# Optimization experiments

Hardware: AMD Instinct MI355X
Metric: run time of the kernel (lower is better)

## Reference

```python
import jax, jax.numpy as jnp
import numpy as np

H = 2048          # hidden_size
I = 2048          # per-expert intermediate = 6144 // (topk=2 + share=1)
E_ROUTED = 7      # num_experts - num_share_experts
NS = 1            # num_share_experts
TOPK = 2
TEMP = 1.0


def setup_inputs() -> dict:
    key = jax.random.key(0)
    ks = jax.random.split(key, 20)
    s = lambda fan_in: 1.0 / np.sqrt(fan_in)
    inp = {
        "x": jax.random.normal(ks[0], (4, 1024, H), dtype=jnp.float32),
        # router (nn.Linear(H, E_ROUTED)) + learnable gate bias (init zeros)
        "Wr": jax.random.normal(ks[1], (H, E_ROUTED), jnp.float32) * s(H),
        "br": jax.random.normal(ks[2], (E_ROUTED,), jnp.float32) * s(H),
        "gate_bias": jnp.zeros((E_ROUTED,), jnp.float32),
        # stacked routed-expert FFN params (up -> SwiGLU gate -> down)
        "Wup": jax.random.normal(ks[3], (E_ROUTED, H, I), jnp.float32) * s(H),
        "bup": jax.random.normal(ks[4], (E_ROUTED, I), jnp.float32) * s(H),
        "Wgate": jax.random.normal(ks[5], (E_ROUTED, I, I), jnp.float32) * s(I),
        "bgate": jax.random.normal(ks[6], (E_ROUTED, I), jnp.float32) * s(I),
        "Wdown": jax.random.normal(ks[7], (E_ROUTED, I, H), jnp.float32) * s(I),
        "bdown": jax.random.normal(ks[8], (E_ROUTED, H), jnp.float32) * s(I),
        # shared expert: share_up Linear(H, NS*I), SwiGLU(I), share_down Linear(I, H)
        "Wsu": jax.random.normal(ks[9], (H, NS * I), jnp.float32) * s(H),
        "bsu": jax.random.normal(ks[10], (NS * I,), jnp.float32) * s(H),
        "Wsg": jax.random.normal(ks[11], (I, I), jnp.float32) * s(I),
        "bsg": jax.random.normal(ks[12], (I,), jnp.float32) * s(I),
        "Wsd": jax.random.normal(ks[13], (I, H), jnp.float32) * s(I),
        "bsd": jax.random.normal(ks[14], (H,), jnp.float32) * s(I),
    }
    return inp


def _moe_forward(x, Wr, br, gate_bias, Wup, bup, Wgate, bgate, Wdown, bdown,
                 Wsu, bsu, Wsg, bsg, Wsd, bsd):
    B, S, _ = x.shape
    xt = x.reshape(-1, H)                                   # [N, H]
    N = xt.shape[0]

    # ---- router: top-k gating with scatter(-inf) + softmax over all routed experts
    gate = (xt @ Wr + br) / TEMP                            # [N, E]
    bias_gate = gate + gate_bias
    _, ids = jax.lax.top_k(bias_gate, TOPK)                 # [N, K]
    sel_logits = jnp.take_along_axis(gate, ids, axis=-1)    # [N, K] (unbiased logits)
    masked = jnp.full_like(gate, -jnp.inf)
    masked = masked.at[jnp.arange(N)[:, None], ids].set(sel_logits)
    probs = jax.nn.softmax(masked, axis=-1)                 # [N, E], zero off top-k

    # ---- routed experts: dense grouped FFN, combine weighted by probs
    # (probs are exactly 0 for unselected experts, matching the masked
    #  gather / scatter-add combine in the original loop)
    u = jnp.einsum('nh,ehi->eni', xt, Wup) + bup[:, None, :]            # [E, N, I]
    g = jax.nn.silu(jnp.einsum('eni,eij->enj', u, Wgate) + bgate[:, None, :]) * u
    eo = jnp.einsum('enj,ejh->enh', g, Wdown) + bdown[:, None, :]       # [E, N, H]
    out = jnp.einsum('ne,enh->nh', probs, eo)                           # [N, H]

    # ---- shared expert(s)
    su = (xt @ Wsu + bsu).reshape(N, NS, I)                 # [N, NS, I]
    sg = jax.nn.silu(su @ Wsg + bsg) * su                   # SwiGLU
    so = (sg @ Wsd + bsd).sum(axis=1)                       # [N, H]
    out = out + so

    return out.reshape(B, S, H)


def reference(x, Wr, br, gate_bias, Wup, bup, Wgate, bgate, Wdown, bdown,
              Wsu, bsu, Wsg, bsg, Wsd, bsd):
    return _moe_forward(x, Wr, br, gate_bias, Wup, bup, Wgate, bgate,
                        Wdown, bdown, Wsu, bsu, Wsg, bsg, Wsd, bsd)
```

## Files before the change

kernel.cpp:

```cpp
#include <hip/hip_runtime.h>
#include <stdint.h>

#define HD 2048
#define NTOK 4096
#define NROUTED 7
#define NEXP 8
#define ROWS_ROUTED 8192
#define ROWS_TOTAL 12288
#define ROWS_PAD 12416

#define BM 256
#define BN 256
#define BK 32
#define NT (HD / BK)

typedef __attribute__((ext_vector_type(8))) __bf16 bf16x8;
typedef __attribute__((ext_vector_type(4))) float f32x4;
typedef __attribute__((ext_vector_type(8))) unsigned short u16x8;

__device__ __forceinline__ float bf2f(unsigned short h) {
  union { unsigned int u; float f; } x; x.u = ((unsigned int)h) << 16; return x.f;
}
__device__ __forceinline__ unsigned short f2bf(float f) {
  union { float f; unsigned int u; } x; x.f = f;
  unsigned int r = x.u + 0x7fffu + ((x.u >> 16) & 1u);
  return (unsigned short)(r >> 16);
}

__device__ __forceinline__ void async16(const void* g, void* l) {
  __builtin_amdgcn_global_load_lds(
      (__attribute__((address_space(1))) const void*)(uintptr_t)g,
      (__attribute__((address_space(3))) void*)(unsigned int)(uintptr_t)l,
      16, 0, 0);
}

__global__ __launch_bounds__(256) void k_convert_bf16(const float* __restrict__ in,
                                                      unsigned short* __restrict__ out, int n) {
  int i = (blockIdx.x * 256 + threadIdx.x) * 4;
  if (i >= n) return;
  float4 v = *(const float4*)(in + i);
  ushort4 o; o.x = f2bf(v.x); o.y = f2bf(v.y); o.z = f2bf(v.z); o.w = f2bf(v.w);
  *(ushort4*)(out + i) = o;
}

__global__ __launch_bounds__(256) void k_transpose_bf16(const float* __restrict__ in,
                                                        unsigned short* __restrict__ out) {
  __shared__ float tile[64][65];
  const size_t bs = (size_t)HD * HD;
  in += (size_t)blockIdx.z * bs; out += (size_t)blockIdx.z * bs;
  int tx = threadIdx.x & 15, ty = threadIdx.x >> 4;
  int r0 = blockIdx.y * 64, c0 = blockIdx.x * 64;
  #pragma unroll
  for (int i = 0; i < 4; i++) {
    float4 v = *(const float4*)(in + (size_t)(r0 + ty + 16 * i) * HD + c0 + tx * 4);
    tile[ty + 16 * i][tx * 4 + 0] = v.x;
    tile[ty + 16 * i][tx * 4 + 1] = v.y;
    tile[ty + 16 * i][tx * 4 + 2] = v.z;
    tile[ty + 16 * i][tx * 4 + 3] = v.w;
  }
  __syncthreads();
  #pragma unroll
  for (int i = 0; i < 4; i++) {
    int orow = ty + 16 * i;
    int oc = tx * 4;
    ushort4 o;
    o.x = f2bf(tile[oc + 0][orow]);
    o.y = f2bf(tile[oc + 1][orow]);
    o.z = f2bf(tile[oc + 2][orow]);
    o.w = f2bf(tile[oc + 3][orow]);
    *(ushort4*)(out + (size_t)(c0 + orow) * HD + r0 + oc) = o;
  }
}

__global__ __launch_bounds__(256) void k_router(const float* __restrict__ x, const float* __restrict__ Wr,
                                                const float* __restrict__ br, const float* __restrict__ gbias,
                                                int* __restrict__ ids, float* __restrict__ wts,
                                                int* __restrict__ ctrl) {
  int lane = threadIdx.x & 63, wid = threadIdx.x >> 6;
  int t = blockIdx.x * 4 + wid;
  const float* xr = x + (size_t)t * HD;
  float acc[NROUTED];
  #pragma unroll
  for (int e = 0; e < NROUTED; e++) acc[e] = 0.f;
  for (int k = lane; k < HD; k += 64) {
    float xv = xr[k];
    const float* wrow = Wr + k * NROUTED;
    #pragma unroll
    for (int e = 0; e < NROUTED; e++) acc[e] += xv * wrow[e];
  }
  #pragma unroll
  for (int e = 0; e < NROUTED; e++) {
    #pragma unroll
    for (int off = 32; off > 0; off >>= 1) acc[e] += __shfl_down(acc[e], off);
  }
  if (lane == 0) {
    float lg[NROUTED], bg[NROUTED];
    #pragma unroll
    for (int e = 0; e < NROUTED; e++) { lg[e] = acc[e] + br[e]; bg[e] = lg[e] + gbias[e]; }
    int i1 = 0;
    #pragma unroll
    for (int e = 1; e < NROUTED; e++) if (bg[e] > bg[i1]) i1 = e;
    int i2 = (i1 == 0) ? 1 : 0;
    #pragma unroll
    for (int e = 0; e < NROUTED; e++) if (e != i1 && bg[e] > bg[i2]) i2 = e;
    float l1 = lg[i1], l2 = lg[i2];
    float m = fmaxf(l1, l2);
    float p1 = __expf(l1 - m), p2 = __expf(l2 - m);
    float s = p1 + p2;
    ids[2*t] = i1; ids[2*t+1] = i2;
    wts[2*t] = p1 / s; wts[2*t+1] = p2 / s;
    atomicAdd(&ctrl[i1], 1); atomicAdd(&ctrl[i2], 1);
  }
}

__global__ void k_offsets(int* ctrl) {
  if (threadIdx.x == 0 && blockIdx.x == 0) {
    ctrl[7] = NTOK;
    int o = 0;
    #pragma unroll
    for (int e = 0; e < NEXP; e++) { ctrl[8 + e] = o; o += ctrl[e]; }
  }
}

__global__ __launch_bounds__(256) void k_build_lists(const int* __restrict__ ids, int* __restrict__ ctrl,
                                                     int* __restrict__ tok_list, int* __restrict__ tok_pos) {
  int t = blockIdx.x * 256 + threadIdx.x;
  if (t >= NTOK) return;
  #pragma unroll
  for (int j = 0; j < 2; j++) {
    int e = ids[2*t + j];
    int pos = ctrl[8 + e] + atomicAdd(&ctrl[16 + e], 1);
    tok_list[pos] = t;
    tok_pos[2*t + j] = pos;
  }
  tok_list[ROWS_ROUTED + t] = t;
}


#define STAGE(bufp)                                                       \
  { unsigned short* _a = &sm[bufp][0][0];                                 \
    unsigned short* _b = &sm[bufp][1][0];                                 \
    _Pragma("unroll")                                                     \
    for (int r = 0; r < 2; r++) {                                         \
      async16(pA[r], _a + r * 4096 + wid * 512); pA[r] += BK;             \
      async16(pB[r], _b + r * 4096 + wid * 512); pB[r] += BK;             \
    } }

template<int MODE>
__global__ __launch_bounds__(512, 2) void k_moe_gemm(
    const unsigned short* __restrict__ Abase,
    const unsigned short* __restrict__ WTr,
    const unsigned short* __restrict__ WTs,
    const float* __restrict__ biasR,
    const float* __restrict__ biasS,
    const int* __restrict__ ctrl,
    const int* __restrict__ tok_list,
    const unsigned short* __restrict__ Uep,
    unsigned short* __restrict__ Out)
{
  const int e   = blockIdx.z;
  const int cnt = ctrl[e];
  const int m0  = blockIdx.y * BM;
  if (m0 >= cnt) return;
  const int off = ctrl[8 + e];
  const int n0  = blockIdx.x * BN;

  const unsigned short* W = (e < NROUTED) ? (WTr + (size_t)e * HD * HD) : WTs;
  const float* bias = (e < NROUTED) ? (biasR + e * HD) : biasS;

  __shared__ __align__(16) unsigned short sm[2][2][BM * BK];

  const int tid  = threadIdx.x;
  const int lane = tid & 63;
  const int wid  = tid >> 6;

  const int sc  = tid & 3;
  const int rl  = tid >> 2;
  const int csw = (sc ^ (rl & 3)) * 8;
  const unsigned short* pA[2];
  const unsigned short* pB[2];
  #pragma unroll
  for (int r = 0; r < 2; r++) {
    int row = r * 128 + rl;
    size_t ga;
    if (MODE == 0) {
      int mr = m0 + row; if (mr >= cnt) mr = cnt - 1;
      ga = (size_t)tok_list[off + mr] * HD;
    } else {
      ga = (size_t)(off + m0 + row) * HD;
    }
    pA[r] = Abase + ga + csw;
    pB[r] = W + (size_t)(n0 + row) * HD + csw;
  }

  const int wr   = wid >> 2;
  const int wc   = wid & 3;
  const int rm   = lane & 15;
  const int q    = lane >> 4;
  const int sw   = rm & 3;
  const int aRow = wr * 128 + rm;
  const int bRow = wc * 64 + rm;

  f32x4 acc[8][4];
  f32x4 zero = {0.f, 0.f, 0.f, 0.f};
  #pragma unroll
  for (int i = 0; i < 8; i++)
    #pragma unroll
    for (int j = 0; j < 4; j++) acc[i][j] = zero;

  STAGE(0);
  __syncthreads();

  for (int t = 0; t < NT; ++t) {
    const int buf = t & 1;
    if (t + 1 < NT) STAGE(buf ^ 1);

    const unsigned short* _ab = &sm[buf][0][0];
    const unsigned short* _bb = &sm[buf][1][0];
    bf16x8 af[8], bf[4];
    #pragma unroll
    for (int mi = 0; mi < 8; mi++)
      af[mi] = *(const bf16x8*)(_ab + (aRow + mi * 16) * BK + ((q ^ sw) * 8));
    #pragma unroll
    for (int ni = 0; ni < 4; ni++)
      bf[ni] = *(const bf16x8*)(_bb + (bRow + ni * 16) * BK + ((q ^ sw) * 8));
    #pragma unroll
    for (int mi = 0; mi < 8; mi++)
      #pragma unroll
      for (int ni = 0; ni < 4; ni++)
        acc[mi][ni] = __builtin_amdgcn_mfma_f32_16x16x32_bf16(af[mi], bf[ni], acc[mi][ni], 0, 0, 0);

    __syncthreads();
  }

  #pragma unroll
  for (int mi = 0; mi < 8; mi++) {
    int rb = wr * 128 + mi * 16 + q * 4;
    #pragma unroll
    for (int r = 0; r < 4; r++) {
      int gm = m0 + rb + r;
      if (gm < cnt) {
        size_t orow = (size_t)(off + gm) * HD;
        #pragma unroll
        for (int ni = 0; ni < 4; ni++) {
          int gn = n0 + wc * 64 + ni * 16 + rm;
          float v = acc[mi][ni][r] + bias[gn];
          if (MODE == 1) {
            float uv = bf2f(Uep[orow + gn]);
            float sg = v / (1.f + __expf(-v));
            v = sg * uv;
          }
          Out[orow + gn] = f2bf(v);
        }
      }
    }
  }
}

__global__ __launch_bounds__(256) void k_combine(const unsigned short* __restrict__ eo,
                                                 const int* __restrict__ tok_pos,
                                                 const float* __restrict__ wts,
                                                 float* __restrict__ out) {
  int t = blockIdx.x;
  int h = threadIdx.x * 8;
  int p0 = tok_pos[2*t], p1 = tok_pos[2*t+1];
  float w0 = wts[2*t], w1 = wts[2*t+1];
  u16x8 a = *(const u16x8*)(eo + (size_t)p0 * HD + h);
  u16x8 b = *(const u16x8*)(eo + (size_t)p1 * HD + h);
  u16x8 c = *(const u16x8*)(eo + (size_t)(ROWS_ROUTED + t) * HD + h);
  float* o = out + (size_t)t * HD + h;
  #pragma unroll
  for (int i = 0; i < 8; i++) o[i] = w0 * bf2f(a[i]) + w1 * bf2f(b[i]) + bf2f(c[i]);
}

extern "C" void kernel_launch(void* const* d_in, const int* in_sizes, int n_in,
                              void* d_out, int out_size, void* d_ws, size_t ws_size,
                              hipStream_t stream) {
  (void)in_sizes; (void)n_in; (void)out_size; (void)ws_size;
  const float* x     = (const float*)d_in[0];
  const float* Wr    = (const float*)d_in[1];
  const float* br    = (const float*)d_in[2];
  const float* gbias = (const float*)d_in[3];
  const float* Wup   = (const float*)d_in[4];
  const float* bup   = (const float*)d_in[5];
  const float* Wgate = (const float*)d_in[6];
  const float* bgate = (const float*)d_in[7];
  const float* Wdown = (const float*)d_in[8];
  const float* bdown = (const float*)d_in[9];
  const float* Wsu   = (const float*)d_in[10];
  const float* bsu   = (const float*)d_in[11];
  const float* Wsg   = (const float*)d_in[12];
  const float* bsg   = (const float*)d_in[13];
  const float* Wsd   = (const float*)d_in[14];
  const float* bsd   = (const float*)d_in[15];
  float* out = (float*)d_out;

  char* ws = (char*)d_ws;
  size_t o = 0;
  auto alloc = [&](size_t bytes) { char* p = ws + o; o += (bytes + 255) & ~(size_t)255; return p; };
  unsigned short* WT_r = (unsigned short*)alloc((size_t)7 * HD * HD * 2);
  unsigned short* WT_s = (unsigned short*)alloc((size_t)HD * HD * 2);
  unsigned short* xbf  = (unsigned short*)alloc((size_t)NTOK * HD * 2);
  unsigned short* bufU = (unsigned short*)alloc((size_t)ROWS_PAD * HD * 2);
  unsigned short* bufG = (unsigned short*)alloc((size_t)ROWS_PAD * HD * 2);
  int*   ctrl     = (int*)alloc(4096);
  int*   ids      = (int*)alloc(NTOK * 2 * 4);
  float* wts      = (float*)alloc(NTOK * 2 * 4);
  int*   tok_list = (int*)alloc(ROWS_TOTAL * 4);
  int*   tok_pos  = (int*)alloc(NTOK * 2 * 4);

  hipMemsetAsync(ctrl, 0, 96, stream);
  k_convert_bf16<<<NTOK * HD / 1024, 256, 0, stream>>>(x, xbf, NTOK * HD);
  k_router<<<NTOK / 4, 256, 0, stream>>>(x, Wr, br, gbias, ids, wts, ctrl);
  k_offsets<<<1, 64, 0, stream>>>(ctrl);
  k_build_lists<<<NTOK / 256, 256, 0, stream>>>(ids, ctrl, tok_list, tok_pos);

  dim3 tgrid(HD / 64, HD / 64, 7), tgrid1(HD / 64, HD / 64, 1);
  dim3 ggrid(HD / BN, 16, NEXP);

  k_transpose_bf16<<<tgrid, 256, 0, stream>>>(Wup, WT_r);
  k_transpose_bf16<<<tgrid1, 256, 0, stream>>>(Wsu, WT_s);
  k_moe_gemm<0><<<ggrid, 512, 0, stream>>>(xbf, WT_r, WT_s, bup, bsu, ctrl, tok_list, nullptr, bufU);

  k_transpose_bf16<<<tgrid, 256, 0, stream>>>(Wgate, WT_r);
  k_transpose_bf16<<<tgrid1, 256, 0, stream>>>(Wsg, WT_s);
  k_moe_gemm<1><<<ggrid, 512, 0, stream>>>(bufU, WT_r, WT_s, bgate, bsg, ctrl, tok_list, bufU, bufG);

  k_transpose_bf16<<<tgrid, 256, 0, stream>>>(Wdown, WT_r);
  k_transpose_bf16<<<tgrid1, 256, 0, stream>>>(Wsd, WT_s);
  k_moe_gemm<2><<<ggrid, 512, 0, stream>>>(bufG, WT_r, WT_s, bdown, bsd, ctrl, tok_list, nullptr, bufU);

  k_combine<<<NTOK, 256, 0, stream>>>(bufU, tok_pos, wts, out);
}
```

Baseline: 1.215 ms.

## Prefetch two tiles ahead with vmcnt waits, new LDS swizzle, merged transposes

New measurement: 1.222 ms. No clear change (+0.6%).

```diff
diff --git a/kernel.cpp b/kernel.cpp
--- a/kernel.cpp
+++ b/kernel.cpp
@@ -43,11 +43,15 @@
   *(ushort4*)(out + i) = o;
 }
 
-__global__ __launch_bounds__(256) void k_transpose_bf16(const float* __restrict__ in,
-                                                        unsigned short* __restrict__ out) {
+__global__ __launch_bounds__(256) void k_transpose_bf16(const float* __restrict__ inR,
+                                                        const float* __restrict__ inS,
+                                                        unsigned short* __restrict__ outR,
+                                                        unsigned short* __restrict__ outS) {
   __shared__ float tile[64][65];
   const size_t bs = (size_t)HD * HD;
-  in += (size_t)blockIdx.z * bs; out += (size_t)blockIdx.z * bs;
+  int z = blockIdx.z;
+  const float* in = (z < NROUTED) ? (inR + (size_t)z * bs) : inS;
+  unsigned short* out = (z < NROUTED) ? (outR + (size_t)z * bs) : outS;
   int tx = threadIdx.x & 15, ty = threadIdx.x >> 4;
   int r0 = blockIdx.y * 64, c0 = blockIdx.x * 64;
   #pragma unroll
@@ -174,14 +178,14 @@
   const int lane = tid & 63;
   const int wid  = tid >> 6;
 
-  const int sc  = tid & 3;
-  const int rl  = tid >> 2;
-  const int csw = (sc ^ (rl & 3)) * 8;
+  const int srow = tid >> 2;
+  const int sslot = tid & 3;
+  const int csw = (sslot ^ ((srow >> 1) & 3)) * 8;
   const unsigned short* pA[2];
   const unsigned short* pB[2];
   #pragma unroll
   for (int r = 0; r < 2; r++) {
-    int row = r * 128 + rl;
+    int row = r * 128 + srow;
     size_t ga;
     if (MODE == 0) {
       int mr = m0 + row; if (mr >= cnt) mr = cnt - 1;
@@ -197,9 +201,7 @@
   const int wc   = wid & 3;
   const int rm   = lane & 15;
   const int q    = lane >> 4;
-  const int sw   = rm & 3;
-  const int aRow = wr * 128 + rm;
-  const int bRow = wc * 64 + rm;
+  const int qx   = (q ^ ((rm >> 1) & 3)) * 8;
 
   f32x4 acc[8][4];
   f32x4 zero = {0.f, 0.f, 0.f, 0.f};
@@ -209,28 +211,34 @@
     for (int j = 0; j < 4; j++) acc[i][j] = zero;
 
   STAGE(0);
-  __syncthreads();
+  STAGE(1);
 
   for (int t = 0; t < NT; ++t) {
     const int buf = t & 1;
-    if (t + 1 < NT) STAGE(buf ^ 1);
+    if (t < NT - 1) { asm volatile("s_waitcnt vmcnt(4)" ::: "memory"); }
+    else           { asm volatile("s_waitcnt vmcnt(0)" ::: "memory"); }
+    __builtin_amdgcn_s_barrier();
+    __builtin_amdgcn_sched_barrier(0);
 
     const unsigned short* _ab = &sm[buf][0][0];
     const unsigned short* _bb = &sm[buf][1][0];
-    bf16x8 af[8], bf[4];
+    bf16x8 af[8], bfr[4];
     #pragma unroll
     for (int mi = 0; mi < 8; mi++)
-      af[mi] = *(const bf16x8*)(_ab + (aRow + mi * 16) * BK + ((q ^ sw) * 8));
+      af[mi] = *(const bf16x8*)(_ab + (wr * 128 + mi * 16 + rm) * BK + qx);
     #pragma unroll
     for (int ni = 0; ni < 4; ni++)
-      bf[ni] = *(const bf16x8*)(_bb + (bRow + ni * 16) * BK + ((q ^ sw) * 8));
+      bfr[ni] = *(const bf16x8*)(_bb + (wc * 64 + ni * 16 + rm) * BK + qx);
     #pragma unroll
     for (int mi = 0; mi < 8; mi++)
       #pragma unroll
       for (int ni = 0; ni < 4; ni++)
-        acc[mi][ni] = __builtin_amdgcn_mfma_f32_16x16x32_bf16(af[mi], bf[ni], acc[mi][ni], 0, 0, 0);
-
-    __syncthreads();
+        acc[mi][ni] = __builtin_amdgcn_mfma_f32_16x16x32_bf16(af[mi], bfr[ni], acc[mi][ni], 0, 0, 0);
+
+    __builtin_amdgcn_sched_barrier(0);
+    __builtin_amdgcn_s_barrier();
+    __builtin_amdgcn_sched_barrier(0);
+    if (t + 2 < NT) STAGE(buf);
   }
 
   #pragma unroll
@@ -315,19 +323,16 @@
   k_offsets<<<1, 64, 0, stream>>>(ctrl);
   k_build_lists<<<NTOK / 256, 256, 0, stream>>>(ids, ctrl, tok_list, tok_pos);
 
-  dim3 tgrid(HD / 64, HD / 64, 7), tgrid1(HD / 64, HD / 64, 1);
-  dim3 ggrid(HD / BN, 16, NEXP);
-
-  k_transpose_bf16<<<tgrid, 256, 0, stream>>>(Wup, WT_r);
-  k_transpose_bf16<<<tgrid1, 256, 0, stream>>>(Wsu, WT_s);
+  dim3 tgrid(HD / 64, HD / 64, NEXP);
+  dim3 ggrid(HD / BN, 4096 / BM, NEXP);
+
+  k_transpose_bf16<<<tgrid, 256, 0, stream>>>(Wup, Wsu, WT_r, WT_s);
   k_moe_gemm<0><<<ggrid, 512, 0, stream>>>(xbf, WT_r, WT_s, bup, bsu, ctrl, tok_list, nullptr, bufU);
 
-  k_transpose_bf16<<<tgrid, 256, 0, stream>>>(Wgate, WT_r);
-  k_transpose_bf16<<<tgrid1, 256, 0, stream>>>(Wsg, WT_s);
+  k_transpose_bf16<<<tgrid, 256, 0, stream>>>(Wgate, Wsg, WT_r, WT_s);
   k_moe_gemm<1><<<ggrid, 512, 0, stream>>>(bufU, WT_r, WT_s, bgate, bsg, ctrl, tok_list, bufU, bufG);
 
-  k_transpose_bf16<<<tgrid, 256, 0, stream>>>(Wdown, WT_r);
-  k_transpose_bf16<<<tgrid1, 256, 0, stream>>>(Wsd, WT_s);
+  k_transpose_bf16<<<tgrid, 256, 0, stream>>>(Wdown, Wsd, WT_r, WT_s);
   k_moe_gemm<2><<<ggrid, 512, 0, stream>>>(bufG, WT_r, WT_s, bdown, bsd, ctrl, tok_list, nullptr, bufU);
 
   k_combine<<<NTOK, 256, 0, stream>>>(bufU, tok_pos, wts, out);
```
